# Performance work log

Hardware: AMD Instinct MI355X
Metric: run time of the kernel (lower is better)

The kernel has to match this reference:

```python
import jax, jax.numpy as jnp
import numpy as np

N_EMBD = 384
BLOCK_SIZE = 256

def setup_inputs() -> dict:
    key = jax.random.key(0)
    k1, k2 = jax.random.split(key)
    B, T = 512, 256
    x = jax.random.normal(k1, (B, T, N_EMBD), dtype=jnp.float32)
    # nn.Linear(384, 192, bias=False): store as [in, out] so projection is x @ w
    w_qkv = jax.random.normal(k2, (N_EMBD, 3 * 64), dtype=jnp.float32) * (1.0 / np.sqrt(N_EMBD))
    return {"x": x, "w_qkv": w_qkv}

def reference(x, w_qkv):
    B, T, C = x.shape  # C == n_embd == 384
    qkv = jnp.einsum('btc,cd->btd', x, w_qkv)       # [B,T,3*hs]
    q, k, v = jnp.split(qkv, 3, axis=-1)            # each [B,T,hs]
    scale = 1.0 / jnp.sqrt(jnp.float32(C))          # NOTE: scales by full embed dim C, per source
    wei = jnp.einsum('btd,bsd->bts', q, k) * scale  # [B,T,T]
    causal = jnp.tril(jnp.ones((T, T), dtype=bool))
    wei = jnp.where(causal, wei, -jnp.inf)
    wei = jax.nn.softmax(wei, axis=-1)
    # dropout is identity in eval mode
    return jnp.einsum('bts,bsd->btd', wei, v)       # [B,T,hs]
```

## Files before the change

kernel.cpp:

```cpp
#include <hip/hip_runtime.h>
#include <hip/hip_bf16.h>


constexpr int B  = 512;
constexpr int T  = 256;
constexpr int C  = 384;
constexpr int HS = 64;
constexpr long BT = (long)B * T;
constexpr long PLANE = BT * HS;
constexpr float SCALE = 0.05103103630798288f;

constexpr int NT   = 192;
constexpr int MT   = 128;
constexpr int BK   = 64;
constexpr int ROWP = 72;
constexpr int VP   = 264;

typedef _Float16 f16x8 __attribute__((ext_vector_type(8)));
typedef _Float16 f16x4 __attribute__((ext_vector_type(4)));
typedef __fp16   fp16x2_raw __attribute__((ext_vector_type(2)));
typedef float    f32x4 __attribute__((ext_vector_type(4)));

__global__ __launch_bounds__(256)
void wt_kernel(const float* __restrict__ w, _Float16* __restrict__ wt) {
    const int idx = blockIdx.x * 256 + threadIdx.x;
    if (idx < NT * C) {
        const int n = idx / C, k = idx % C;
        wt[idx] = (_Float16)w[k * NT + n];
    }
}

__global__ __launch_bounds__(256)
void proj_kernel(const float* __restrict__ x, const _Float16* __restrict__ wt,
                 _Float16* __restrict__ qp, _Float16* __restrict__ kp,
                 _Float16* __restrict__ vtp) {
    __shared__ __align__(16) _Float16 XL[MT * ROWP];
    __shared__ __align__(16) _Float16 WL[NT * ROWP];

    const int tid  = threadIdx.x;
    const int lane = tid & 63;
    const int wv   = tid >> 6;
    const int wm   = wv >> 1, wn = wv & 1;
    const int l15  = lane & 15, quad = lane >> 4;
    const long row0 = (long)blockIdx.x * MT;

    f32x4 acc[4][6];
#pragma unroll
    for (int mi = 0; mi < 4; ++mi)
#pragma unroll
        for (int ni = 0; ni < 6; ++ni) acc[mi][ni] = (f32x4)0.f;

    for (int kc = 0; kc < C / BK; ++kc) {
        const int k0 = kc * BK;
        __syncthreads();
#pragma unroll
        for (int i = 0; i < 8; ++i) {
            const int flat = tid + 256 * i;
            const int r = flat >> 4, seg = flat & 15;
            const float4 xv = *(const float4*)(x + (row0 + r) * C + k0 + seg * 4);
            union { fp16x2_raw h[2]; uint2 u; } cvt;
            cvt.h[0] = __builtin_amdgcn_cvt_pkrtz(xv.x, xv.y);
            cvt.h[1] = __builtin_amdgcn_cvt_pkrtz(xv.z, xv.w);
            *(uint2*)&XL[r * ROWP + seg * 4] = cvt.u;
        }
#pragma unroll
        for (int i = 0; i < 6; ++i) {
            const int flat = tid + 256 * i;
            const int n = flat >> 3, seg = flat & 7;
            *(uint4*)&WL[n * ROWP + seg * 8] = *(const uint4*)(wt + n * C + k0 + seg * 8);
        }
        __syncthreads();

#pragma unroll
        for (int s = 0; s < 2; ++s) {
            const int kk = s * 32 + quad * 8;
            f16x8 a[4], bfr[6];
#pragma unroll
            for (int mi = 0; mi < 4; ++mi)
                a[mi] = *(const f16x8*)&XL[(wm * 64 + mi * 16 + l15) * ROWP + kk];
#pragma unroll
            for (int ni = 0; ni < 6; ++ni)
                bfr[ni] = *(const f16x8*)&WL[(wn * 96 + ni * 16 + l15) * ROWP + kk];
#pragma unroll
            for (int mi = 0; mi < 4; ++mi)
#pragma unroll
                for (int ni = 0; ni < 6; ++ni)
                    acc[mi][ni] = __builtin_amdgcn_mfma_f32_16x16x32_f16(
                        a[mi], bfr[ni], acc[mi][ni], 0, 0, 0);
        }
    }

#pragma unroll
    for (int mi = 0; mi < 4; ++mi) {
        const long grow0 = row0 + wm * 64 + mi * 16 + quad * 4;
        const int bb = (int)(grow0 >> 8);
        const int t0 = (int)(grow0 & 255);
#pragma unroll
        for (int ni = 0; ni < 6; ++ni) {
            const int colbase = wn * 96 + ni * 16;
            const int col = colbase + l15;
            if (colbase < 64) {
#pragma unroll
                for (int r = 0; r < 4; ++r)
                    qp[(grow0 + r) * HS + col] = (_Float16)acc[mi][ni][r];
            } else if (colbase < 128) {
#pragma unroll
                for (int r = 0; r < 4; ++r)
                    kp[(grow0 + r) * HS + (col - 64)] = (_Float16)acc[mi][ni][r];
            } else {
                f16x4 pv;
#pragma unroll
                for (int r = 0; r < 4; ++r) pv[r] = (_Float16)acc[mi][ni][r];
                *(f16x4*)&vtp[(long)bb * (HS * T) + (col - 128) * T + t0] = pv;
            }
        }
    }
}

__global__ __launch_bounds__(256)
void attn_kernel(const _Float16* __restrict__ qp, const _Float16* __restrict__ kp,
                 const _Float16* __restrict__ vtp, float* __restrict__ out) {
    __shared__ __align__(16) _Float16 VL[HS * VP];

    const int b = blockIdx.x, tid = threadIdx.x;
    const int lane = tid & 63, w = tid >> 6;
    const int l15 = lane & 15, quad = lane >> 4;

    const _Float16* Vg = vtp + (long)b * (HS * T);
#pragma unroll
    for (int i = 0; i < 8; ++i) {
        const int flat = tid + 256 * i;
        const int r = flat >> 5, seg = flat & 31;
        *(uint4*)&VL[r * VP + seg * 8] = *(const uint4*)(Vg + r * T + seg * 8);
    }
    __syncthreads();

    const _Float16* Qg = qp + ((long)b * T + w * 64) * HS;
    const _Float16* Kg = kp + (long)b * T * HS;
    f16x8 qf[4][2];
#pragma unroll
    for (int ni = 0; ni < 4; ++ni)
#pragma unroll
        for (int ks = 0; ks < 2; ++ks)
            qf[ni][ks] = *(const f16x8*)(Qg + (ni * 16 + l15) * HS + ks * 32 + quad * 8);

    f32x4 o[4][4];
#pragma unroll
    for (int di = 0; di < 4; ++di)
#pragma unroll
        for (int ni = 0; ni < 4; ++ni) o[di][ni] = (f32x4)0.f;
    float lp[4] = {0.f, 0.f, 0.f, 0.f};

    for (int c = 0; c <= w; ++c) {
        const bool diag = (c == w);
#pragma unroll
        for (int kt = 0; kt < 4; ++kt) {
            const int key0 = c * 64 + kt * 16;
            const f16x8 ka0 = *(const f16x8*)(Kg + (key0 + l15) * HS + quad * 8);
            const f16x8 ka1 = *(const f16x8*)(Kg + (key0 + l15) * HS + 32 + quad * 8);
            f16x4 va[4];
#pragma unroll
            for (int di = 0; di < 4; ++di)
                va[di] = *(const f16x4*)&VL[(di * 16 + l15) * VP + key0 + quad * 4];
#pragma unroll
            for (int ni = 0; ni < 4; ++ni) {
                if (diag && kt > ni) continue;
                f32x4 s = {0.f, 0.f, 0.f, 0.f};
                s = __builtin_amdgcn_mfma_f32_16x16x32_f16(ka0, qf[ni][0], s, 0, 0, 0);
                s = __builtin_amdgcn_mfma_f32_16x16x32_f16(ka1, qf[ni][1], s, 0, 0, 0);
                const bool dmask = diag && (kt == ni);
                f16x4 pb;
                float psum = 0.f;
#pragma unroll
                for (int r = 0; r < 4; ++r) {
                    float pr = __expf(s[r] * SCALE);
                    pr = (dmask && (quad * 4 + r > l15)) ? 0.f : pr;
                    psum += pr;
                    pb[r] = (_Float16)pr;
                }
                lp[ni] += psum;
#pragma unroll
                for (int di = 0; di < 4; ++di)
                    o[di][ni] = __builtin_amdgcn_mfma_f32_16x16x16f16(
                        va[di], pb, o[di][ni], 0, 0, 0);
            }
        }
    }

#pragma unroll
    for (int ni = 0; ni < 4; ++ni) {
        float v = lp[ni];
        v += __shfl_xor(v, 16, 64);
        v += __shfl_xor(v, 32, 64);
        lp[ni] = 1.0f / v;
    }

    float* ob = out + ((long)b * T + w * 64) * HS;
#pragma unroll
    for (int ni = 0; ni < 4; ++ni)
#pragma unroll
        for (int di = 0; di < 4; ++di) {
            float4 val;
            val.x = o[di][ni][0] * lp[ni];
            val.y = o[di][ni][1] * lp[ni];
            val.z = o[di][ni][2] * lp[ni];
            val.w = o[di][ni][3] * lp[ni];
            *(float4*)&ob[(ni * 16 + l15) * HS + di * 16 + quad * 4] = val;
        }
}

extern "C" void kernel_launch(void* const* d_in, const int* in_sizes, int n_in,
                              void* d_out, int out_size, void* d_ws, size_t ws_size,
                              hipStream_t stream) {
    const float* x = (const float*)d_in[0];
    const float* w = (const float*)d_in[1];
    float* out = (float*)d_out;

    _Float16* qp  = (_Float16*)d_ws;
    _Float16* kp  = qp + PLANE;
    _Float16* vtp = kp + PLANE;
    _Float16* wt  = vtp + PLANE;

    wt_kernel<<<dim3((NT * C + 255) / 256), dim3(256), 0, stream>>>(w, wt);
    proj_kernel<<<dim3((unsigned)(BT / MT)), dim3(256), 0, stream>>>(x, wt, qp, kp, vtp);
    attn_kernel<<<dim3(B), dim3(256), 0, stream>>>(qp, kp, vtp, out);
}
```

Before: 323.5 us.

## Balance causal attention across 8 waves and prefetch projection tiles into registers

The attention kernel now runs 8 waves per batch, and each wave owns two 16-row query strips paired as (i, 15-i). This evens out the causal triangle work across waves, where before the last wave did four times the work of the first. The projection kernel prefetches the next x chunk and the current weight chunk into registers before the barrier, so global load latency can overlap the LDS stores and MFMA work. This adds register pressure in both kernels, and the attention kernel now has 512 threads per block.

```diff
diff --git a/kernel.cpp b/kernel.cpp
--- a/kernel.cpp
+++ b/kernel.cpp
@@ -50,24 +50,46 @@
 #pragma unroll
         for (int ni = 0; ni < 6; ++ni) acc[mi][ni] = (f32x4)0.f;
 
+    float4 xr[8];
+#pragma unroll
+    for (int i = 0; i < 8; ++i) {
+        const int flat = tid + 256 * i;
+        const int r = flat >> 4, seg = flat & 15;
+        xr[i] = *(const float4*)(x + (row0 + r) * C + seg * 4);
+    }
+
     for (int kc = 0; kc < C / BK; ++kc) {
         const int k0 = kc * BK;
+        uint4 wr[6];
+#pragma unroll
+        for (int i = 0; i < 6; ++i) {
+            const int flat = tid + 256 * i;
+            const int n = flat >> 3, seg = flat & 7;
+            wr[i] = *(const uint4*)(wt + n * C + k0 + seg * 8);
+        }
         __syncthreads();
 #pragma unroll
         for (int i = 0; i < 8; ++i) {
             const int flat = tid + 256 * i;
             const int r = flat >> 4, seg = flat & 15;
-            const float4 xv = *(const float4*)(x + (row0 + r) * C + k0 + seg * 4);
-            union { fp16x2_raw h[2]; uint2 u; } cvt;
-            cvt.h[0] = __builtin_amdgcn_cvt_pkrtz(xv.x, xv.y);
-            cvt.h[1] = __builtin_amdgcn_cvt_pkrtz(xv.z, xv.w);
-            *(uint2*)&XL[r * ROWP + seg * 4] = cvt.u;
+            union { fp16x2_raw h[2]; uint2 u; } cv;
+            cv.h[0] = __builtin_amdgcn_cvt_pkrtz(xr[i].x, xr[i].y);
+            cv.h[1] = __builtin_amdgcn_cvt_pkrtz(xr[i].z, xr[i].w);
+            *(uint2*)&XL[r * ROWP + seg * 4] = cv.u;
         }
 #pragma unroll
         for (int i = 0; i < 6; ++i) {
             const int flat = tid + 256 * i;
             const int n = flat >> 3, seg = flat & 7;
-            *(uint4*)&WL[n * ROWP + seg * 8] = *(const uint4*)(wt + n * C + k0 + seg * 8);
+            *(uint4*)&WL[n * ROWP + seg * 8] = wr[i];
+        }
+        if (kc < C / BK - 1) {
+#pragma unroll
+            for (int i = 0; i < 8; ++i) {
+                const int flat = tid + 256 * i;
+                const int r = flat >> 4, seg = flat & 15;
+                xr[i] = *(const float4*)(x + (row0 + r) * C + k0 + BK + seg * 4);
+            }
         }
         __syncthreads();
 
@@ -117,96 +139,100 @@
     }
 }
 
-__global__ __launch_bounds__(256)
+__global__ __launch_bounds__(512)
 void attn_kernel(const _Float16* __restrict__ qp, const _Float16* __restrict__ kp,
                  const _Float16* __restrict__ vtp, float* __restrict__ out) {
     __shared__ __align__(16) _Float16 VL[HS * VP];
 
     const int b = blockIdx.x, tid = threadIdx.x;
-    const int lane = tid & 63, w = tid >> 6;
+    const int lane = tid & 63, wv = tid >> 6;
     const int l15 = lane & 15, quad = lane >> 4;
 
     const _Float16* Vg = vtp + (long)b * (HS * T);
 #pragma unroll
-    for (int i = 0; i < 8; ++i) {
-        const int flat = tid + 256 * i;
+    for (int i = 0; i < 4; ++i) {
+        const int flat = tid + 512 * i;
         const int r = flat >> 5, seg = flat & 31;
         *(uint4*)&VL[r * VP + seg * 8] = *(const uint4*)(Vg + r * T + seg * 8);
     }
     __syncthreads();
 
-    const _Float16* Qg = qp + ((long)b * T + w * 64) * HS;
+    const int s0 = wv, s1 = 15 - wv;
+    const _Float16* Qg = qp + (long)b * T * HS;
     const _Float16* Kg = kp + (long)b * T * HS;
-    f16x8 qf[4][2];
-#pragma unroll
-    for (int ni = 0; ni < 4; ++ni)
-#pragma unroll
-        for (int ks = 0; ks < 2; ++ks)
-            qf[ni][ks] = *(const f16x8*)(Qg + (ni * 16 + l15) * HS + ks * 32 + quad * 8);
-
-    f32x4 o[4][4];
-#pragma unroll
-    for (int di = 0; di < 4; ++di)
-#pragma unroll
-        for (int ni = 0; ni < 4; ++ni) o[di][ni] = (f32x4)0.f;
-    float lp[4] = {0.f, 0.f, 0.f, 0.f};
-
-    for (int c = 0; c <= w; ++c) {
-        const bool diag = (c == w);
-#pragma unroll
-        for (int kt = 0; kt < 4; ++kt) {
-            const int key0 = c * 64 + kt * 16;
-            const f16x8 ka0 = *(const f16x8*)(Kg + (key0 + l15) * HS + quad * 8);
-            const f16x8 ka1 = *(const f16x8*)(Kg + (key0 + l15) * HS + 32 + quad * 8);
-            f16x4 va[4];
+
+    f16x8 qf0[2], qf1[2];
+#pragma unroll
+    for (int ks = 0; ks < 2; ++ks) {
+        qf0[ks] = *(const f16x8*)(Qg + (s0 * 16 + l15) * HS + ks * 32 + quad * 8);
+        qf1[ks] = *(const f16x8*)(Qg + (s1 * 16 + l15) * HS + ks * 32 + quad * 8);
+    }
+
+    f32x4 o0[4], o1[4];
+#pragma unroll
+    for (int di = 0; di < 4; ++di) { o0[di] = (f32x4)0.f; o1[di] = (f32x4)0.f; }
+    float lp0 = 0.f, lp1 = 0.f;
+
+    for (int kt = 0; kt <= s1; ++kt) {
+        const int key0 = kt * 16;
+        const f16x8 ka0 = *(const f16x8*)(Kg + (key0 + l15) * HS + quad * 8);
+        const f16x8 ka1 = *(const f16x8*)(Kg + (key0 + l15) * HS + 32 + quad * 8);
+        f16x4 va[4];
+#pragma unroll
+        for (int di = 0; di < 4; ++di)
+            va[di] = *(const f16x4*)&VL[(di * 16 + l15) * VP + key0 + quad * 4];
+
+        {
+            f32x4 s = {0.f, 0.f, 0.f, 0.f};
+            s = __builtin_amdgcn_mfma_f32_16x16x32_f16(ka0, qf1[0], s, 0, 0, 0);
+            s = __builtin_amdgcn_mfma_f32_16x16x32_f16(ka1, qf1[1], s, 0, 0, 0);
+            const bool dm = (kt == s1);
+            f16x4 pb; float ps = 0.f;
+#pragma unroll
+            for (int r = 0; r < 4; ++r) {
+                float pr = __expf(s[r] * SCALE);
+                pr = (dm && (quad * 4 + r > l15)) ? 0.f : pr;
+                ps += pr; pb[r] = (_Float16)pr;
+            }
+            lp1 += ps;
 #pragma unroll
             for (int di = 0; di < 4; ++di)
-                va[di] = *(const f16x4*)&VL[(di * 16 + l15) * VP + key0 + quad * 4];
-#pragma unroll
-            for (int ni = 0; ni < 4; ++ni) {
-                if (diag && kt > ni) continue;
-                f32x4 s = {0.f, 0.f, 0.f, 0.f};
-                s = __builtin_amdgcn_mfma_f32_16x16x32_f16(ka0, qf[ni][0], s, 0, 0, 0);
-                s = __builtin_amdgcn_mfma_f32_16x16x32_f16(ka1, qf[ni][1], s, 0, 0, 0);
-                const bool dmask = diag && (kt == ni);
-                f16x4 pb;
-                float psum = 0.f;
-#pragma unroll
-                for (int r = 0; r < 4; ++r) {
-                    float pr = __expf(s[r] * SCALE);
-                    pr = (dmask && (quad * 4 + r > l15)) ? 0.f : pr;
-                    psum += pr;
-                    pb[r] = (_Float16)pr;
-                }
-                lp[ni] += psum;
-#pragma unroll
-                for (int di = 0; di < 4; ++di)
-                    o[di][ni] = __builtin_amdgcn_mfma_f32_16x16x16f16(
-                        va[di], pb, o[di][ni], 0, 0, 0);
-            }
-        }
-    }
-
-#pragma unroll
-    for (int ni = 0; ni < 4; ++ni) {
-        float v = lp[ni];
-        v += __shfl_xor(v, 16, 64);
-        v += __shfl_xor(v, 32, 64);
-        lp[ni] = 1.0f / v;
-    }
-
-    float* ob = out + ((long)b * T + w * 64) * HS;
-#pragma unroll
-    for (int ni = 0; ni < 4; ++ni)
-#pragma unroll
-        for (int di = 0; di < 4; ++di) {
-            float4 val;
-            val.x = o[di][ni][0] * lp[ni];
-            val.y = o[di][ni][1] * lp[ni];
-            val.z = o[di][ni][2] * lp[ni];
-            val.w = o[di][ni][3] * lp[ni];
-            *(float4*)&ob[(ni * 16 + l15) * HS + di * 16 + quad * 4] = val;
-        }
+                o1[di] = __builtin_amdgcn_mfma_f32_16x16x16f16(va[di], pb, o1[di], 0, 0, 0);
+        }
+        if (kt <= s0) {
+            f32x4 s = {0.f, 0.f, 0.f, 0.f};
+            s = __builtin_amdgcn_mfma_f32_16x16x32_f16(ka0, qf0[0], s, 0, 0, 0);
+            s = __builtin_amdgcn_mfma_f32_16x16x32_f16(ka1, qf0[1], s, 0, 0, 0);
+            const bool dm = (kt == s0);
+            f16x4 pb; float ps = 0.f;
+#pragma unroll
+            for (int r = 0; r < 4; ++r) {
+                float pr = __expf(s[r] * SCALE);
+                pr = (dm && (quad * 4 + r > l15)) ? 0.f : pr;
+                ps += pr; pb[r] = (_Float16)pr;
+            }
+            lp0 += ps;
+#pragma unroll
+            for (int di = 0; di < 4; ++di)
+                o0[di] = __builtin_amdgcn_mfma_f32_16x16x16f16(va[di], pb, o0[di], 0, 0, 0);
+        }
+    }
+
+    lp0 += __shfl_xor(lp0, 16, 64); lp0 += __shfl_xor(lp0, 32, 64);
+    lp1 += __shfl_xor(lp1, 16, 64); lp1 += __shfl_xor(lp1, 32, 64);
+    const float i0 = 1.0f / lp0, i1 = 1.0f / lp1;
+
+    float* ob = out + (long)b * T * HS;
+#pragma unroll
+    for (int di = 0; di < 4; ++di) {
+        float4 v0, v1;
+        v0.x = o0[di][0] * i0; v0.y = o0[di][1] * i0;
+        v0.z = o0[di][2] * i0; v0.w = o0[di][3] * i0;
+        v1.x = o1[di][0] * i1; v1.y = o1[di][1] * i1;
+        v1.z = o1[di][2] * i1; v1.w = o1[di][3] * i1;
+        *(float4*)&ob[(s0 * 16 + l15) * HS + di * 16 + quad * 4] = v0;
+        *(float4*)&ob[(s1 * 16 + l15) * HS + di * 16 + quad * 4] = v1;
+    }
 }
 
 extern "C" void kernel_launch(void* const* d_in, const int* in_sizes, int n_in,
@@ -223,5 +249,5 @@
 
     wt_kernel<<<dim3((NT * C + 255) / 256), dim3(256), 0, stream>>>(w, wt);
     proj_kernel<<<dim3((unsigned)(BT / MT)), dim3(256), 0, stream>>>(x, wt, qp, kp, vtp);
-    attn_kernel<<<dim3(B), dim3(256), 0, stream>>>(qp, kp, vtp, out);
-}
+    attn_kernel<<<dim3(B), dim3(512), 0, stream>>>(qp, kp, vtp, out);
+}
```

Measured after the change: 333.1 us. 3.0% more time.
